# Kernel tuning notes

Measured on AMD Instinct MI355X. Metric: run time of the kernel, lower is better.

Reference implementation:

```python
import jax, jax.numpy as jnp
import numpy as np
import math

IN_CH = 256
OUT_CH = 256
N_JOINTS = 25
BATCH = 16384


def setup_inputs() -> dict:
    key = jax.random.key(0)
    kx, kw = jax.random.split(key)
    x = jax.random.normal(kx, (N_JOINTS, BATCH, IN_CH), dtype=jnp.float32)
    stdv = 1.0 / math.sqrt(OUT_CH)
    weight = jax.random.uniform(kw, (IN_CH, OUT_CH), dtype=jnp.float32,
                                minval=-stdv, maxval=stdv)
    return {"x": x, "weight": weight}


def reference(x, weight):
    # x: (N, B, D) -> attention over joints N per batch element
    xb = jnp.transpose(x, (1, 0, 2))            # (B, N, D)
    s3 = jnp.einsum('bnd,bmd->bnm', xb, xb)     # (B, N, N) self-similarity
    s = jax.nn.softmax(s3, axis=-1)
    out = jnp.einsum('bnm,bmd->bnd', s, xb)     # (B, N, D)
    out = out @ weight                           # (B, N, out_channels)
    return out
```

## Files before the change

kernel.cpp:

```cpp
#include <hip/hip_runtime.h>

#define GRID   1024
#define BLOCK  256
#define BATCH  16384
#define NJ     25
#define DEPTH  256
#define ITERS  (BATCH / GRID)

typedef short s16x8 __attribute__((ext_vector_type(8)));
typedef short s16x4 __attribute__((ext_vector_type(4)));
typedef float f32x4 __attribute__((ext_vector_type(4)));

__device__ __forceinline__ short f2bf(float f) {
  union { float f; unsigned u; } c; c.f = f;
  unsigned r = (c.u + 0x7FFFu + ((c.u >> 16) & 1u)) >> 16;
  return (short)r;
}

#define MFMA(a, b, c) __builtin_amdgcn_mfma_f32_16x16x32_bf16((a), (b), (c), 0, 0, 0)

__global__ __launch_bounds__(BLOCK, 2)
void geo_gcn_fused(const float* __restrict__ x,
                   const float* __restrict__ w,
                   float* __restrict__ out)
{
  __shared__ short As[2][32][256];
  __shared__ short Ps[32][40];
  __shared__ float S3[32][33];
  __shared__ short Yt[4][64][40];

  const int tid  = threadIdx.x;
  const int wv   = tid >> 6;
  const int lane = tid & 63;
  const int quad = lane >> 4;
  const int l16  = lane & 15;

  s16x8 wf[8][4];
  {
    const int ncol = wv * 64 + l16;
#pragma unroll
    for (int ks = 0; ks < 8; ++ks)
#pragma unroll
      for (int td = 0; td < 4; ++td) {
        const float* wp = w + (size_t)(ks * 32 + quad * 8) * DEPTH + ncol + td * 16;
#pragma unroll
        for (int j = 0; j < 8; ++j)
          wf[ks][td][j] = f2bf(wp[(size_t)j * DEPTH]);
      }
  }

  const int tm_s = wv >> 1;
  const int tn_s = wv & 1;
  const int srow = tid >> 3;
  const int sq   = tid & 7;
  const int ssw  = (sq ^ (srow & 7)) * 8;

  const float* xb = x + (size_t)srow * BATCH * DEPTH + sq * 8;

  {
    const float* xp = xb + (size_t)blockIdx.x * DEPTH;
#pragma unroll
    for (int c = 0; c < 4; ++c) {
      float4 c0 = make_float4(0.f, 0.f, 0.f, 0.f), c1 = c0;
      if (srow < NJ) {
        c0 = *(const float4*)(xp + c * 64);
        c1 = *(const float4*)(xp + c * 64 + 4);
      }
      s16x8 h;
      h[0]=f2bf(c0.x); h[1]=f2bf(c0.y); h[2]=f2bf(c0.z); h[3]=f2bf(c0.w);
      h[4]=f2bf(c1.x); h[5]=f2bf(c1.y); h[6]=f2bf(c1.z); h[7]=f2bf(c1.w);
      *(s16x8*)&As[0][srow][ssw + c * 64] = h;
    }
  }
  __syncthreads();

  for (int ib = 0; ib < ITERS; ++ib) {
    const int b   = blockIdx.x + GRID * ib;
    const int buf = ib & 1;

    float4 nf[8];
#pragma unroll
    for (int i = 0; i < 8; ++i) nf[i] = make_float4(0.f, 0.f, 0.f, 0.f);
    if ((ib + 1 < ITERS) && (srow < NJ)) {
      const float* xp = xb + (size_t)(b + GRID) * DEPTH;
#pragma unroll
      for (int c = 0; c < 4; ++c) {
        nf[2 * c]     = *(const float4*)(xp + c * 64);
        nf[2 * c + 1] = *(const float4*)(xp + c * 64 + 4);
      }
    }

    f32x4 sacc = (f32x4){0.f, 0.f, 0.f, 0.f};
    f32x4 yacc[2][4];
#pragma unroll
    for (int i = 0; i < 2; ++i)
#pragma unroll
      for (int j = 0; j < 4; ++j) yacc[i][j] = (f32x4){0.f, 0.f, 0.f, 0.f};

#pragma unroll
    for (int ks = 0; ks < 8; ++ks) {
      const int co = (((ks * 4 + quad) ^ (l16 & 7)) << 3);
      s16x8 a0 = *(const s16x8*)&As[buf][l16][co];
      s16x8 a1 = *(const s16x8*)&As[buf][16 + l16][co];
      sacc = MFMA(tm_s ? a1 : a0, tn_s ? a1 : a0, sacc);
#pragma unroll
      for (int td = 0; td < 4; ++td) {
        yacc[0][td] = MFMA(a0, wf[ks][td], yacc[0][td]);
        yacc[1][td] = MFMA(a1, wf[ks][td], yacc[1][td]);
      }
    }

#pragma unroll
    for (int r = 0; r < 4; ++r)
      S3[tm_s * 16 + quad * 4 + r][tn_s * 16 + l16] = sacc[r];
    __syncthreads();

    {
      const int row = tid >> 3, c8 = tid & 7;
      float v[4]; float mx = -3.0e38f;
#pragma unroll
      for (int i = 0; i < 4; ++i) {
        const int j = c8 + 8 * i;
        v[i] = (j < NJ) ? S3[row][j] : -3.0e38f;
        mx = fmaxf(mx, v[i]);
      }
      mx = fmaxf(mx, __shfl_xor(mx, 1));
      mx = fmaxf(mx, __shfl_xor(mx, 2));
      mx = fmaxf(mx, __shfl_xor(mx, 4));
      float e[4]; float sum = 0.f;
#pragma unroll
      for (int i = 0; i < 4; ++i) {
        const int j = c8 + 8 * i;
        e[i] = (j < NJ) ? __expf(v[i] - mx) : 0.f;
        sum += e[i];
      }
      sum += __shfl_xor(sum, 1);
      sum += __shfl_xor(sum, 2);
      sum += __shfl_xor(sum, 4);
      const float rinv = 1.0f / sum;
#pragma unroll
      for (int i = 0; i < 4; ++i)
        Ps[row][c8 + 8 * i] = f2bf(e[i] * rinv);
    }

    if (ib + 1 < ITERS) {
#pragma unroll
      for (int c = 0; c < 4; ++c) {
        s16x8 h;
        h[0]=f2bf(nf[2*c].x);   h[1]=f2bf(nf[2*c].y);
        h[2]=f2bf(nf[2*c].z);   h[3]=f2bf(nf[2*c].w);
        h[4]=f2bf(nf[2*c+1].x); h[5]=f2bf(nf[2*c+1].y);
        h[6]=f2bf(nf[2*c+1].z); h[7]=f2bf(nf[2*c+1].w);
        *(s16x8*)&As[1 - buf][srow][ssw + c * 64] = h;
      }
    }
    __syncthreads();

#pragma unroll
    for (int tm = 0; tm < 2; ++tm)
#pragma unroll
      for (int td = 0; td < 4; ++td) {
        s16x4 hy;
#pragma unroll
        for (int r = 0; r < 4; ++r) hy[r] = f2bf(yacc[tm][td][r]);
        *(s16x4*)&Yt[wv][td * 16 + l16][tm * 16 + quad * 4] = hy;
      }

    s16x8 pf0 = *(const s16x8*)&Ps[l16][quad * 8];
    s16x8 pf1 = *(const s16x8*)&Ps[16 + l16][quad * 8];
    const f32x4 z4 = (f32x4){0.f, 0.f, 0.f, 0.f};
    float* ob = out + (size_t)b * NJ * DEPTH + wv * 64 + l16;
#pragma unroll
    for (int td = 0; td < 4; ++td) {
      s16x8 yb = *(const s16x8*)&Yt[wv][td * 16 + l16][quad * 8];
      f32x4 o0 = MFMA(pf0, yb, z4);
      f32x4 o1 = MFMA(pf1, yb, z4);
#pragma unroll
      for (int r = 0; r < 4; ++r) {
        ob[(size_t)(quad * 4 + r) * DEPTH + td * 16] = o0[r];
        const int nr = 16 + quad * 4 + r;
        if (nr < NJ) ob[(size_t)nr * DEPTH + td * 16] = o1[r];
      }
    }
  }
}

extern "C" void kernel_launch(void* const* d_in, const int* in_sizes, int n_in,
                              void* d_out, int out_size, void* d_ws, size_t ws_size,
                              hipStream_t stream) {
  (void)in_sizes; (void)n_in; (void)out_size; (void)d_ws; (void)ws_size;
  const float* x = (const float*)d_in[0];
  const float* w = (const float*)d_in[1];
  float* out = (float*)d_out;
  geo_gcn_fused<<<dim3(GRID), dim3(BLOCK), 0, stream>>>(x, w, out);
}
```

Measured before the change: 712.4 us.

## Compute softmax redundantly per wave in MFMA layout, drop a barrier, swizzle Yt

```diff
diff --git a/kernel.cpp b/kernel.cpp
--- a/kernel.cpp
+++ b/kernel.cpp
@@ -25,9 +25,8 @@
                    float* __restrict__ out)
 {
   __shared__ short As[2][32][256];
-  __shared__ short Ps[32][40];
-  __shared__ float S3[32][33];
-  __shared__ short Yt[4][64][40];
+  __shared__ float S3[2][32][36];
+  __shared__ short Yt[4][64][32];
 
   const int tid  = threadIdx.x;
   const int wv   = tid >> 6;
@@ -112,36 +111,7 @@
 
 #pragma unroll
     for (int r = 0; r < 4; ++r)
-      S3[tm_s * 16 + quad * 4 + r][tn_s * 16 + l16] = sacc[r];
-    __syncthreads();
-
-    {
-      const int row = tid >> 3, c8 = tid & 7;
-      float v[4]; float mx = -3.0e38f;
-#pragma unroll
-      for (int i = 0; i < 4; ++i) {
-        const int j = c8 + 8 * i;
-        v[i] = (j < NJ) ? S3[row][j] : -3.0e38f;
-        mx = fmaxf(mx, v[i]);
-      }
-      mx = fmaxf(mx, __shfl_xor(mx, 1));
-      mx = fmaxf(mx, __shfl_xor(mx, 2));
-      mx = fmaxf(mx, __shfl_xor(mx, 4));
-      float e[4]; float sum = 0.f;
-#pragma unroll
-      for (int i = 0; i < 4; ++i) {
-        const int j = c8 + 8 * i;
-        e[i] = (j < NJ) ? __expf(v[i] - mx) : 0.f;
-        sum += e[i];
-      }
-      sum += __shfl_xor(sum, 1);
-      sum += __shfl_xor(sum, 2);
-      sum += __shfl_xor(sum, 4);
-      const float rinv = 1.0f / sum;
-#pragma unroll
-      for (int i = 0; i < 4; ++i)
-        Ps[row][c8 + 8 * i] = f2bf(e[i] * rinv);
-    }
+      S3[buf][tm_s * 16 + quad * 4 + r][tn_s * 16 + l16] = sacc[r];
 
     if (ib + 1 < ITERS) {
 #pragma unroll
@@ -156,6 +126,51 @@
     }
     __syncthreads();
 
+    s16x8 pf0, pf1;
+    {
+      f32x4 v0a = *(const f32x4*)&S3[buf][l16][quad * 8];
+      f32x4 v0b = *(const f32x4*)&S3[buf][l16][quad * 8 + 4];
+      f32x4 v1a = *(const f32x4*)&S3[buf][16 + l16][quad * 8];
+      f32x4 v1b = *(const f32x4*)&S3[buf][16 + l16][quad * 8 + 4];
+      const float NINF = -3.0e38f;
+      float mx0 = NINF, mx1 = NINF;
+#pragma unroll
+      for (int j = 0; j < 4; ++j) {
+        const bool va = (quad * 8 + j) < NJ;
+        const bool vb = (quad * 8 + 4 + j) < NJ;
+        mx0 = fmaxf(mx0, va ? v0a[j] : NINF);
+        mx0 = fmaxf(mx0, vb ? v0b[j] : NINF);
+        mx1 = fmaxf(mx1, va ? v1a[j] : NINF);
+        mx1 = fmaxf(mx1, vb ? v1b[j] : NINF);
+      }
+      mx0 = fmaxf(mx0, __shfl_xor(mx0, 16));
+      mx0 = fmaxf(mx0, __shfl_xor(mx0, 32));
+      mx1 = fmaxf(mx1, __shfl_xor(mx1, 16));
+      mx1 = fmaxf(mx1, __shfl_xor(mx1, 32));
+      float e0[8], e1[8], s0 = 0.f, s1 = 0.f;
+#pragma unroll
+      for (int j = 0; j < 4; ++j) {
+        const bool va = (quad * 8 + j) < NJ;
+        const bool vb = (quad * 8 + 4 + j) < NJ;
+        e0[j]     = va ? __expf(v0a[j] - mx0) : 0.f;
+        e0[j + 4] = vb ? __expf(v0b[j] - mx0) : 0.f;
+        e1[j]     = va ? __expf(v1a[j] - mx1) : 0.f;
+        e1[j + 4] = vb ? __expf(v1b[j] - mx1) : 0.f;
+        s0 += e0[j] + e0[j + 4];
+        s1 += e1[j] + e1[j + 4];
+      }
+      s0 += __shfl_xor(s0, 16);
+      s0 += __shfl_xor(s0, 32);
+      s1 += __shfl_xor(s1, 16);
+      s1 += __shfl_xor(s1, 32);
+      const float r0 = 1.0f / s0, r1 = 1.0f / s1;
+#pragma unroll
+      for (int j = 0; j < 8; ++j) {
+        pf0[j] = f2bf(e0[j] * r0);
+        pf1[j] = f2bf(e1[j] * r1);
+      }
+    }
+
 #pragma unroll
     for (int tm = 0; tm < 2; ++tm)
 #pragma unroll
@@ -163,23 +178,24 @@
         s16x4 hy;
 #pragma unroll
         for (int r = 0; r < 4; ++r) hy[r] = f2bf(yacc[tm][td][r]);
-        *(s16x4*)&Yt[wv][td * 16 + l16][tm * 16 + quad * 4] = hy;
-      }
-
-    s16x8 pf0 = *(const s16x8*)&Ps[l16][quad * 8];
-    s16x8 pf1 = *(const s16x8*)&Ps[16 + l16][quad * 8];
+        const int pc = (tm * 2 + (quad >> 1)) ^ ((l16 >> 1) & 3);
+        *(s16x4*)&Yt[wv][td * 16 + l16][pc * 8 + (quad & 1) * 4] = hy;
+      }
+
     const f32x4 z4 = (f32x4){0.f, 0.f, 0.f, 0.f};
     float* ob = out + (size_t)b * NJ * DEPTH + wv * 64 + l16;
 #pragma unroll
     for (int td = 0; td < 4; ++td) {
-      s16x8 yb = *(const s16x8*)&Yt[wv][td * 16 + l16][quad * 8];
+      const int pr = quad ^ ((l16 >> 1) & 3);
+      s16x8 yb = *(const s16x8*)&Yt[wv][td * 16 + l16][pr * 8];
       f32x4 o0 = MFMA(pf0, yb, z4);
       f32x4 o1 = MFMA(pf1, yb, z4);
 #pragma unroll
       for (int r = 0; r < 4; ++r) {
-        ob[(size_t)(quad * 4 + r) * DEPTH + td * 16] = o0[r];
+        __builtin_nontemporal_store(o0[r], &ob[(size_t)(quad * 4 + r) * DEPTH + td * 16]);
         const int nr = 16 + quad * 4 + r;
-        if (nr < NJ) ob[(size_t)nr * DEPTH + td * 16] = o1[r];
+        if (nr < NJ)
+          __builtin_nontemporal_store(o1[r], &ob[(size_t)nr * DEPTH + td * 16]);
       }
     }
   }
```

After: 753.2 us. 1.06x slower.
